# Performance work log

Measured on AMD Instinct MI355X. Metric: run time of the kernel, lower is better.

## Reference

```python
import jax, jax.numpy as jnp
import numpy as np

# Model dims
B, S, D = 1, 768, 256          # batch, seq_len, d_model
H, KD = 8, 256                 # num_heads, key_dim
DH = KD // H                   # head_dim = 32
BS, NR, W, G = 64, 3, 3, 1     # block_size, num_rand_blocks, window_size, global_tokens
NEG = -1e9


def _build_sparse_indices(seed=0):
    """Replicates _create_sparse_attention_mask (sparse branch) with numpy.
    Returns (attn_indices [S, M] int32 clamped >=0, blocked_mask [1,1,S,M] float32)."""
    nb = S // BS  # num_blocks (S divisible by BS here)
    rng = np.random.RandomState(seed)
    r = np.arange(nb)
    # window pairs |i - j| <= W
    ii, jj = np.meshgrid(r, r, indexing='ij')
    win = np.abs(ii - jj) <= W
    window_pairs = np.stack([ii[win], jj[win]], axis=1)
    # global: every block -> first G blocks; first G blocks -> every block
    g = np.arange(G)
    glob_to = np.stack([np.repeat(r, G), np.tile(g, nb)], axis=1)
    glob_from = np.stack([np.repeat(g, nb), np.tile(r, G)], axis=1)
    # random pairs
    rand_pairs = rng.randint(0, nb, size=(NR * nb, 2))
    allp = np.concatenate([window_pairs, glob_to, glob_from, rand_pairs], axis=0)
    uniq = np.unique(allp[:, 0] * nb + allp[:, 1])  # sorted unique (row, col)
    rows, cols = uniq // nb, uniq % nb
    max_row = int(np.max(np.bincount(rows, minlength=nb)))
    M = max_row * BS  # padded neighbor-token width (= S when a global block is dense)
    idx = np.full((nb, M), -1, dtype=np.int64)
    for b in range(nb):
        cs = cols[rows == b]
        toks = (cs[:, None] * BS + np.arange(BS)[None, :]).reshape(-1)
        idx[b, :toks.size] = toks
    tok_idx = idx[np.arange(S) // BS]  # expand per-block rows to per-token rows [S, M]
    mask = np.where(tok_idx >= 0, 0.0, NEG).astype(np.float32)
    return np.maximum(tok_idx, 0).astype(np.int32), mask[None, None]


def setup_inputs() -> dict:
    key = jax.random.key(0)
    ks = jax.random.split(key, 8)

    def dense_w(k, fi, fo):  # glorot-uniform like keras Dense
        lim = float(np.sqrt(6.0 / (fi + fo)))
        return jax.random.uniform(k, (fi, fo), jnp.float32, -lim, lim)

    attn_indices, blocked_mask = _build_sparse_indices()
    return {
        'query': jax.random.normal(ks[0], (B, S, D), jnp.float32),
        'value': jax.random.normal(ks[1], (B, S, D), jnp.float32),
        'key_in': jax.random.normal(ks[2], (B, S, D), jnp.float32),
        'Wq': dense_w(ks[3], D, KD), 'bq': jnp.zeros((KD,), jnp.float32),
        'Wk': dense_w(ks[4], D, KD), 'bk': jnp.zeros((KD,), jnp.float32),
        'Wv': dense_w(ks[5], D, KD), 'bv': jnp.zeros((KD,), jnp.float32),
        'Wo': dense_w(ks[6], KD, D), 'bo': jnp.zeros((D,), jnp.float32),
        'attn_indices': jnp.asarray(attn_indices),
        'blocked_mask': jnp.asarray(blocked_mask),
    }


def reference(query, value, key_in, Wq, bq, Wk, bk, Wv, bv, Wo, bo, attn_indices, blocked_mask):
    q = query @ Wq + bq
    k = key_in @ Wk + bk
    v = value @ Wv + bv

    def split_heads(x):  # [B,S,KD] -> [B*H,S,DH]
        return x.reshape(B, S, H, DH).transpose(0, 2, 1, 3).reshape(B * H, S, DH)

    q = split_heads(q) * (DH ** -0.5)
    k = split_heads(k)
    v = split_heads(v)

    # gather sparse neighbor tokens (indices shared across batch*heads)
    k_g = jnp.take(k, attn_indices, axis=1)  # [BH, S, M, DH]
    v_g = jnp.take(v, attn_indices, axis=1)  # [BH, S, M, DH]

    scores = jnp.einsum('bnd,bnmd->bnm', q, k_g)  # [BH, S, M]
    M = attn_indices.shape[1]
    scores = scores.reshape(B, H, S, M) + blocked_mask  # pad positions -> -1e9
    probs = jax.nn.softmax(scores, axis=-1)

    ctx = jnp.einsum('bnm,bnmd->bnd', probs.reshape(B * H, S, M), v_g)  # [BH,S,DH]
    ctx = ctx.reshape(B, H, S, DH).transpose(0, 2, 1, 3).reshape(B, S, KD)
    out = ctx @ Wo + bo
    return out, scores, attn_indices
```

## Files before the change

### kernel.cpp

```cpp
#include <hip/hip_runtime.h>
#include <math.h>

#define SQ 768
#define DMODEL 256
#define NH 8
#define DHD 32
#define NB 12
#define QSCALE 0.1767766952966369f
#define PSHIFT 8.0f

__global__ __launch_bounds__(256) void proj3(
    const float* __restrict__ query, const float* __restrict__ value,
    const float* __restrict__ key_in,
    const float* __restrict__ Wq, const float* __restrict__ bq,
    const float* __restrict__ Wk, const float* __restrict__ bk,
    const float* __restrict__ Wv, const float* __restrict__ bv,
    const float* __restrict__ bo, float* __restrict__ outbuf,
    const int* __restrict__ aidx, float* __restrict__ idx_out,
    float* __restrict__ qhp, float* __restrict__ khp, float* __restrict__ vhp)
{
    const int j = threadIdx.x;

    {
        const int bidf = blockIdx.y * 192 + blockIdx.x;
        const int i0 = (bidf * 256 + j) * 4;
        int4 v = *(const int4*)&aidx[i0];
        *(float4*)&idx_out[i0] =
            make_float4((float)v.x, (float)v.y, (float)v.z, (float)v.w);
    }

    const int s0 = blockIdx.x * 4;
    const int w  = blockIdx.y;

    if (w == 0) {
        const float bb = bo[j];
        #pragma unroll
        for (int r = 0; r < 4; ++r)
            outbuf[(s0 + r) * DMODEL + j] = bb;
    }

    const float *X, *W, *bias; float* out; float scale;
    if (w == 0)      { X = query;  W = Wq; bias = bq; out = qhp; scale = QSCALE; }
    else if (w == 1) { X = key_in; W = Wk; bias = bk; out = khp; scale = 1.0f; }
    else             { X = value;  W = Wv; bias = bv; out = vhp; scale = 1.0f; }

    __shared__ float xs[4][DMODEL];
    for (int i = j; i < 4 * DMODEL; i += 256)
        xs[i >> 8][i & 255] = X[s0 * DMODEL + i];
    __syncthreads();

    float acc[4] = {};
    #pragma unroll 4
    for (int k = 0; k < DMODEL; ++k) {
        const float wv = W[k * DMODEL + j];
        #pragma unroll
        for (int r = 0; r < 4; ++r)
            acc[r] = fmaf(xs[r][k], wv, acc[r]);
    }
    const float bb = bias[j];
    const int h = j >> 5, d = j & 31;
    #pragma unroll
    for (int r = 0; r < 4; ++r)
        out[h * (SQ * DHD) + (s0 + r) * DHD + d] = (acc[r] + bb) * scale;
}

__global__ __launch_bounds__(512) void attn2(
    const float* __restrict__ qh, const float* __restrict__ kh,
    const float* __restrict__ vh, const int* __restrict__ aidx,
    const float* __restrict__ mask, const float* __restrict__ Wo,
    float* __restrict__ scores_out, float* __restrict__ out, int M)
{
    __shared__ __align__(16) float Qs[32][33];
    __shared__ __align__(16) float Ks[2][32][68];
    __shared__ __align__(16) float Ps[2][64][33];
    __shared__ __align__(16) float Vs[2][64][36];
    __shared__ float invL[32];

    const int b    = blockIdx.x;
    const int half = blockIdx.y;
    const int h    = blockIdx.z;
    const int s0b  = b * 64;
    const int s0   = s0b + half * 32;
    const int tid  = threadIdx.x;
    const int u    = tid >> 8;
    const int utid = tid & 255;
    const int NCH  = M / 64;

    #pragma unroll
    for (int g = 0; g < 2; ++g) {
        const int idx = tid + g * 512;
        const int r = idx >> 5, d = idx & 31;
        Qs[d][r] = qh[(h * SQ + s0 + r) * DHD + d];
    }

    float4 acc = make_float4(0.f, 0.f, 0.f, 0.f);
    float rps = 0.f;
    const int pr  = utid & 31;
    const int pd  = (utid >> 5) * 4;
    const int qrt = (utid & 15) * 2;
    const int qct = (utid >> 4) * 4;

    for (int ci = 0; ci < NCH / 2; ++ci) {
        const int ch = u * (NCH / 2) + ci;
        const int m0 = ch * 64;
        const float maskv = mask[s0b * M + m0];
        const bool valid = maskv > -0.5f;

        __syncthreads();
        if (valid) {
            const int t0 = aidx[s0b * M + m0];
            const int c = utid & 63;
            #pragma unroll
            for (int g = 0; g < 2; ++g) {
                const int d4 = ((utid >> 6) + g * 4) * 4;
                float4 kv = *(const float4*)&kh[(h * SQ + t0 + c) * DHD + d4];
                Ks[u][d4 + 0][c] = kv.x; Ks[u][d4 + 1][c] = kv.y;
                Ks[u][d4 + 2][c] = kv.z; Ks[u][d4 + 3][c] = kv.w;
                *(float4*)&Vs[u][c][d4] =
                    *(const float4*)&vh[(h * SQ + t0 + c) * DHD + d4];
            }
        } else if (utid < 32) {
            float dt = 0.f;
            #pragma unroll
            for (int d = 0; d < 32; ++d)
                dt = fmaf(Qs[d][utid], kh[h * SQ * DHD + d], dt);
            Ps[u][0][utid] = dt;
        }
        __syncthreads();

        if (valid) {
            float sc[2][4] = {};
            #pragma unroll
            for (int kk = 0; kk < 32; ++kk) {
                const float a0 = Qs[kk][qrt];
                const float a1 = Qs[kk][qrt + 1];
                float4 b4 = *(const float4*)&Ks[u][kk][qct];
                sc[0][0] = fmaf(a0, b4.x, sc[0][0]);
                sc[0][1] = fmaf(a0, b4.y, sc[0][1]);
                sc[0][2] = fmaf(a0, b4.z, sc[0][2]);
                sc[0][3] = fmaf(a0, b4.w, sc[0][3]);
                sc[1][0] = fmaf(a1, b4.x, sc[1][0]);
                sc[1][1] = fmaf(a1, b4.y, sc[1][1]);
                sc[1][2] = fmaf(a1, b4.z, sc[1][2]);
                sc[1][3] = fmaf(a1, b4.w, sc[1][3]);
            }
            #pragma unroll
            for (int i = 0; i < 2; ++i) {
                *(float4*)&scores_out[(h * SQ + s0 + qrt + i) * M + m0 + qct] =
                    make_float4(sc[i][0], sc[i][1], sc[i][2], sc[i][3]);
                #pragma unroll
                for (int jj = 0; jj < 4; ++jj)
                    Ps[u][qct + jj][qrt + i] = __expf(sc[i][jj] - PSHIFT);
            }
        } else {
            const float dv = maskv;
            #pragma unroll
            for (int i = 0; i < 8; ++i) {
                const int e = utid + i * 256;
                const int r = e >> 6, cc = e & 63;
                scores_out[(h * SQ + s0 + r) * M + m0 + cc] = Ps[u][0][r] + dv;
            }
        }
        __syncthreads();

        if (valid) {
            #pragma unroll 4
            for (int c = 0; c < 64; ++c) {
                const float p = Ps[u][c][pr];
                float4 v = *(const float4*)&Vs[u][c][pd];
                acc.x = fmaf(p, v.x, acc.x);
                acc.y = fmaf(p, v.y, acc.y);
                acc.z = fmaf(p, v.z, acc.z);
                acc.w = fmaf(p, v.w, acc.w);
                if (utid < 32) rps += p;
            }
        }
    }

    __syncthreads();
    *(float4*)&Vs[u][pr][pd] = acc;
    if (utid < 32) (&Ps[1][0][0])[u * 32 + utid] = rps;
    __syncthreads();

    if (tid < 32) {
        const float pt = (&Ps[1][0][0])[tid] + (&Ps[1][0][0])[32 + tid];
        invL[tid] = 1.0f / pt;
    }
    __syncthreads();

    float* ctxn = &Ks[0][0][0];
    #pragma unroll
    for (int g = 0; g < 2; ++g) {
        const int idx = tid + g * 512;
        const int r = idx >> 5, d = idx & 31;
        ctxn[r * 36 + d] = (Vs[0][r][d] + Vs[1][r][d]) * invL[r];
    }
    __syncthreads();

    {
        const int jc = tid & 255, rg = tid >> 8;
        float wo[32];
        #pragma unroll
        for (int k = 0; k < 32; ++k)
            wo[k] = Wo[(h * DHD + k) * DMODEL + jc];
        for (int rr = rg * 16; rr < rg * 16 + 16; ++rr) {
            float a = 0.f;
            #pragma unroll
            for (int k4 = 0; k4 < 8; ++k4) {
                float4 cv = *(const float4*)&ctxn[rr * 36 + k4 * 4];
                a = fmaf(cv.x, wo[k4 * 4 + 0], a);
                a = fmaf(cv.y, wo[k4 * 4 + 1], a);
                a = fmaf(cv.z, wo[k4 * 4 + 2], a);
                a = fmaf(cv.w, wo[k4 * 4 + 3], a);
            }
            atomicAdd(&out[(s0 + rr) * DMODEL + jc], a);
        }
    }
}

extern "C" void kernel_launch(void* const* d_in, const int* in_sizes, int n_in,
                              void* d_out, int out_size, void* d_ws, size_t ws_size,
                              hipStream_t stream)
{
    const float* query  = (const float*)d_in[0];
    const float* value  = (const float*)d_in[1];
    const float* key_in = (const float*)d_in[2];
    const float* Wq = (const float*)d_in[3];
    const float* bq = (const float*)d_in[4];
    const float* Wk = (const float*)d_in[5];
    const float* bk = (const float*)d_in[6];
    const float* Wv = (const float*)d_in[7];
    const float* bv = (const float*)d_in[8];
    const float* Wo = (const float*)d_in[9];
    const float* bo = (const float*)d_in[10];
    const int*   aidx = (const int*)d_in[11];
    const float* mask = (const float*)d_in[12];

    const int M = in_sizes[11] / SQ;

    float* out        = (float*)d_out;
    float* scores_out = out + SQ * DMODEL;
    float* idx_out    = scores_out + NH * SQ * M;

    float* ws  = (float*)d_ws;
    float* qhp = ws;
    float* khp = qhp + NH * SQ * DHD;
    float* vhp = khp + NH * SQ * DHD;

    proj3<<<dim3(192, 3), 256, 0, stream>>>(
        query, value, key_in, Wq, bq, Wk, bk, Wv, bv,
        bo, out, aidx, idx_out, qhp, khp, vhp);

    attn2<<<dim3(NB, 2, NH), 512, 0, stream>>>(
        qhp, khp, vhp, aidx, mask, Wo, scores_out, out, M);
}
```

Before: 56.54 us.

## Double-buffer K/V chunks in attention, hold Q in registers, widen projection rows

The attention kernel now prefetches the next 64-token K/V chunk into registers while the current chunk is computed, with double-buffered shared memory, and drops one barrier per chunk. Q rows move from shared memory into registers, and the padded-row dot product is computed once up front. The projection kernel processes 8 rows per block, reading X directly as float4 from global instead of staging it in shared memory, which halves the grid. This raises register pressure and leaves fewer, larger projection blocks, which may hurt occupancy.

After: 75.82 us. 1.34x slower.

```diff
diff --git a/kernel.cpp b/kernel.cpp
--- a/kernel.cpp
+++ b/kernel.cpp
@@ -22,46 +22,53 @@
     const int j = threadIdx.x;
 
     {
-        const int bidf = blockIdx.y * 192 + blockIdx.x;
-        const int i0 = (bidf * 256 + j) * 4;
-        int4 v = *(const int4*)&aidx[i0];
+        const int bidf = blockIdx.y * 96 + blockIdx.x;
+        const int i0 = (bidf * 256 + j) * 8;
+        int4 a = *(const int4*)&aidx[i0];
+        int4 b = *(const int4*)&aidx[i0 + 4];
         *(float4*)&idx_out[i0] =
-            make_float4((float)v.x, (float)v.y, (float)v.z, (float)v.w);
-    }
-
-    const int s0 = blockIdx.x * 4;
+            make_float4((float)a.x, (float)a.y, (float)a.z, (float)a.w);
+        *(float4*)&idx_out[i0 + 4] =
+            make_float4((float)b.x, (float)b.y, (float)b.z, (float)b.w);
+    }
+
+    const int s0 = blockIdx.x * 8;
     const int w  = blockIdx.y;
 
     if (w == 0) {
         const float bb = bo[j];
         #pragma unroll
-        for (int r = 0; r < 4; ++r)
+        for (int r = 0; r < 8; ++r)
             outbuf[(s0 + r) * DMODEL + j] = bb;
     }
 
-    const float *X, *W, *bias; float* out; float scale;
-    if (w == 0)      { X = query;  W = Wq; bias = bq; out = qhp; scale = QSCALE; }
-    else if (w == 1) { X = key_in; W = Wk; bias = bk; out = khp; scale = 1.0f; }
-    else             { X = value;  W = Wv; bias = bv; out = vhp; scale = 1.0f; }
-
-    __shared__ float xs[4][DMODEL];
-    for (int i = j; i < 4 * DMODEL; i += 256)
-        xs[i >> 8][i & 255] = X[s0 * DMODEL + i];
-    __syncthreads();
-
-    float acc[4] = {};
-    #pragma unroll 4
-    for (int k = 0; k < DMODEL; ++k) {
-        const float wv = W[k * DMODEL + j];
-        #pragma unroll
-        for (int r = 0; r < 4; ++r)
-            acc[r] = fmaf(xs[r][k], wv, acc[r]);
+    const float *X, *W, *bias; float* outp; float scale;
+    if (w == 0)      { X = query;  W = Wq; bias = bq; outp = qhp; scale = QSCALE; }
+    else if (w == 1) { X = key_in; W = Wk; bias = bk; outp = khp; scale = 1.0f; }
+    else             { X = value;  W = Wv; bias = bv; outp = vhp; scale = 1.0f; }
+
+    const float4* Xv = (const float4*)(X + s0 * DMODEL);
+    float acc[8] = {};
+    for (int k4 = 0; k4 < DMODEL / 4; ++k4) {
+        float xr[8][4];
+        #pragma unroll
+        for (int r = 0; r < 8; ++r) {
+            float4 t = Xv[r * (DMODEL / 4) + k4];
+            xr[r][0] = t.x; xr[r][1] = t.y; xr[r][2] = t.z; xr[r][3] = t.w;
+        }
+        #pragma unroll
+        for (int kk = 0; kk < 4; ++kk) {
+            const float wv = W[(k4 * 4 + kk) * DMODEL + j];
+            #pragma unroll
+            for (int r = 0; r < 8; ++r)
+                acc[r] = fmaf(xr[r][kk], wv, acc[r]);
+        }
     }
     const float bb = bias[j];
     const int h = j >> 5, d = j & 31;
     #pragma unroll
-    for (int r = 0; r < 4; ++r)
-        out[h * (SQ * DHD) + (s0 + r) * DHD + d] = (acc[r] + bb) * scale;
+    for (int r = 0; r < 8; ++r)
+        outp[h * (SQ * DHD) + (s0 + r) * DHD + d] = (acc[r] + bb) * scale;
 }
 
 __global__ __launch_bounds__(512) void attn2(
@@ -70,10 +77,10 @@
     const float* __restrict__ mask, const float* __restrict__ Wo,
     float* __restrict__ scores_out, float* __restrict__ out, int M)
 {
-    __shared__ __align__(16) float Qs[32][33];
-    __shared__ __align__(16) float Ks[2][32][68];
+    __shared__ __align__(16) float Ks[2][2][32][68];
+    __shared__ __align__(16) float Vs[2][2][64][36];
     __shared__ __align__(16) float Ps[2][64][33];
-    __shared__ __align__(16) float Vs[2][64][36];
+    __shared__ float dot0s[32];
     __shared__ float invL[32];
 
     const int b    = blockIdx.x;
@@ -84,90 +91,134 @@
     const int tid  = threadIdx.x;
     const int u    = tid >> 8;
     const int utid = tid & 255;
-    const int NCH  = M / 64;
-
-    #pragma unroll
-    for (int g = 0; g < 2; ++g) {
-        const int idx = tid + g * 512;
-        const int r = idx >> 5, d = idx & 31;
-        Qs[d][r] = qh[(h * SQ + s0 + r) * DHD + d];
-    }
+    const int NCH2 = M / 128;
+
+    const int qrt = (utid & 15) * 2;
+    const int qct = (utid >> 4) * 4;
+    const int pr  = utid & 31;
+    const int pd  = (utid >> 5) * 4;
+    const int c   = utid & 63;
+    const int dg  = utid >> 6;
+    const int d4a = dg * 4;
+    const int d4b = 16 + dg * 4;
+
+    const float* mrow = &mask[s0b * M];
+    const int*   arow = &aidx[s0b * M];
+    float*       srow = &scores_out[(h * SQ + s0) * M];
+
+    float qr0[32], qr1[32];
+    {
+        const float* qp = &qh[(h * SQ + s0 + qrt) * DHD];
+        #pragma unroll
+        for (int d4 = 0; d4 < DHD; d4 += 4) {
+            float4 a  = *(const float4*)&qp[d4];
+            float4 b4 = *(const float4*)&qp[DHD + d4];
+            qr0[d4] = a.x;  qr0[d4+1] = a.y;  qr0[d4+2] = a.z;  qr0[d4+3] = a.w;
+            qr1[d4] = b4.x; qr1[d4+1] = b4.y; qr1[d4+2] = b4.z; qr1[d4+3] = b4.w;
+        }
+    }
+
+    if (tid < 16) {
+        const float* k0 = &kh[h * SQ * DHD];
+        float a0 = 0.f, a1 = 0.f;
+        #pragma unroll
+        for (int d = 0; d < DHD; ++d) {
+            const float kv = k0[d];
+            a0 = fmaf(qr0[d], kv, a0);
+            a1 = fmaf(qr1[d], kv, a1);
+        }
+        dot0s[qrt] = a0; dot0s[qrt + 1] = a1;
+    }
+
+    float mv_cur = mrow[(u * NCH2) * 64];
+    bool  val_cur = mv_cur > -0.5f;
+    if (val_cur) {
+        const int t0 = arow[(u * NCH2) * 64];
+        const float* kp = &kh[(h * SQ + t0 + c) * DHD];
+        const float* vp = &vh[(h * SQ + t0 + c) * DHD];
+        float4 ka = *(const float4*)&kp[d4a];
+        float4 kb = *(const float4*)&kp[d4b];
+        Ks[u][0][d4a+0][c] = ka.x; Ks[u][0][d4a+1][c] = ka.y;
+        Ks[u][0][d4a+2][c] = ka.z; Ks[u][0][d4a+3][c] = ka.w;
+        Ks[u][0][d4b+0][c] = kb.x; Ks[u][0][d4b+1][c] = kb.y;
+        Ks[u][0][d4b+2][c] = kb.z; Ks[u][0][d4b+3][c] = kb.w;
+        *(float4*)&Vs[u][0][c][d4a] = *(const float4*)&vp[d4a];
+        *(float4*)&Vs[u][0][c][d4b] = *(const float4*)&vp[d4b];
+    }
+    __syncthreads();
 
     float4 acc = make_float4(0.f, 0.f, 0.f, 0.f);
     float rps = 0.f;
-    const int pr  = utid & 31;
-    const int pd  = (utid >> 5) * 4;
-    const int qrt = (utid & 15) * 2;
-    const int qct = (utid >> 4) * 4;
-
-    for (int ci = 0; ci < NCH / 2; ++ci) {
-        const int ch = u * (NCH / 2) + ci;
-        const int m0 = ch * 64;
-        const float maskv = mask[s0b * M + m0];
-        const bool valid = maskv > -0.5f;
-
-        __syncthreads();
-        if (valid) {
-            const int t0 = aidx[s0b * M + m0];
-            const int c = utid & 63;
-            #pragma unroll
-            for (int g = 0; g < 2; ++g) {
-                const int d4 = ((utid >> 6) + g * 4) * 4;
-                float4 kv = *(const float4*)&kh[(h * SQ + t0 + c) * DHD + d4];
-                Ks[u][d4 + 0][c] = kv.x; Ks[u][d4 + 1][c] = kv.y;
-                Ks[u][d4 + 2][c] = kv.z; Ks[u][d4 + 3][c] = kv.w;
-                *(float4*)&Vs[u][c][d4] =
-                    *(const float4*)&vh[(h * SQ + t0 + c) * DHD + d4];
-            }
-        } else if (utid < 32) {
-            float dt = 0.f;
-            #pragma unroll
-            for (int d = 0; d < 32; ++d)
-                dt = fmaf(Qs[d][utid], kh[h * SQ * DHD + d], dt);
-            Ps[u][0][utid] = dt;
-        }
-        __syncthreads();
-
-        if (valid) {
+    int cur = 0;
+
+    for (int ci = 0; ci < NCH2; ++ci) {
+        const int m0 = (u * NCH2 + ci) * 64;
+
+        bool  val_nxt = false;
+        float mv_nxt  = 0.f;
+        float4 ka, kb, va, vb;
+        if (ci + 1 < NCH2) {
+            mv_nxt  = mrow[m0 + 64];
+            val_nxt = mv_nxt > -0.5f;
+            if (val_nxt) {
+                const int t0 = arow[m0 + 64];
+                const float* kp = &kh[(h * SQ + t0 + c) * DHD];
+                const float* vp = &vh[(h * SQ + t0 + c) * DHD];
+                ka = *(const float4*)&kp[d4a];
+                kb = *(const float4*)&kp[d4b];
+                va = *(const float4*)&vp[d4a];
+                vb = *(const float4*)&vp[d4b];
+            }
+        }
+
+        if (val_cur) {
+            const float* Kb = &Ks[u][cur][0][qct];
             float sc[2][4] = {};
             #pragma unroll
             for (int kk = 0; kk < 32; ++kk) {
-                const float a0 = Qs[kk][qrt];
-                const float a1 = Qs[kk][qrt + 1];
-                float4 b4 = *(const float4*)&Ks[u][kk][qct];
-                sc[0][0] = fmaf(a0, b4.x, sc[0][0]);
-                sc[0][1] = fmaf(a0, b4.y, sc[0][1]);
-                sc[0][2] = fmaf(a0, b4.z, sc[0][2]);
-                sc[0][3] = fmaf(a0, b4.w, sc[0][3]);
-                sc[1][0] = fmaf(a1, b4.x, sc[1][0]);
-                sc[1][1] = fmaf(a1, b4.y, sc[1][1]);
-                sc[1][2] = fmaf(a1, b4.z, sc[1][2]);
-                sc[1][3] = fmaf(a1, b4.w, sc[1][3]);
+                float4 b4 = *(const float4*)&Kb[kk * 68];
+                sc[0][0] = fmaf(qr0[kk], b4.x, sc[0][0]);
+                sc[0][1] = fmaf(qr0[kk], b4.y, sc[0][1]);
+                sc[0][2] = fmaf(qr0[kk], b4.z, sc[0][2]);
+                sc[0][3] = fmaf(qr0[kk], b4.w, sc[0][3]);
+                sc[1][0] = fmaf(qr1[kk], b4.x, sc[1][0]);
+                sc[1][1] = fmaf(qr1[kk], b4.y, sc[1][1]);
+                sc[1][2] = fmaf(qr1[kk], b4.z, sc[1][2]);
+                sc[1][3] = fmaf(qr1[kk], b4.w, sc[1][3]);
             }
             #pragma unroll
             for (int i = 0; i < 2; ++i) {
-                *(float4*)&scores_out[(h * SQ + s0 + qrt + i) * M + m0 + qct] =
+                *(float4*)&srow[(qrt + i) * M + m0 + qct] =
                     make_float4(sc[i][0], sc[i][1], sc[i][2], sc[i][3]);
                 #pragma unroll
                 for (int jj = 0; jj < 4; ++jj)
                     Ps[u][qct + jj][qrt + i] = __expf(sc[i][jj] - PSHIFT);
             }
         } else {
-            const float dv = maskv;
             #pragma unroll
             for (int i = 0; i < 8; ++i) {
                 const int e = utid + i * 256;
                 const int r = e >> 6, cc = e & 63;
-                scores_out[(h * SQ + s0 + r) * M + m0 + cc] = Ps[u][0][r] + dv;
-            }
+                srow[r * M + m0 + cc] = dot0s[r] + mv_cur;
+            }
+        }
+
+        if (val_nxt) {
+            Ks[u][cur^1][d4a+0][c] = ka.x; Ks[u][cur^1][d4a+1][c] = ka.y;
+            Ks[u][cur^1][d4a+2][c] = ka.z; Ks[u][cur^1][d4a+3][c] = ka.w;
+            Ks[u][cur^1][d4b+0][c] = kb.x; Ks[u][cur^1][d4b+1][c] = kb.y;
+            Ks[u][cur^1][d4b+2][c] = kb.z; Ks[u][cur^1][d4b+3][c] = kb.w;
+            *(float4*)&Vs[u][cur^1][c][d4a] = va;
+            *(float4*)&Vs[u][cur^1][c][d4b] = vb;
         }
         __syncthreads();
 
-        if (valid) {
+        if (val_cur) {
+            const float (*Vb)[36] = Vs[u][cur];
             #pragma unroll 4
-            for (int c = 0; c < 64; ++c) {
-                const float p = Ps[u][c][pr];
-                float4 v = *(const float4*)&Vs[u][c][pd];
+            for (int cc2 = 0; cc2 < 64; ++cc2) {
+                const float p = Ps[u][cc2][pr];
+                float4 v = *(const float4*)&Vb[cc2][pd];
                 acc.x = fmaf(p, v.x, acc.x);
                 acc.y = fmaf(p, v.y, acc.y);
                 acc.z = fmaf(p, v.z, acc.z);
@@ -175,10 +226,12 @@
                 if (utid < 32) rps += p;
             }
         }
-    }
-
-    __syncthreads();
-    *(float4*)&Vs[u][pr][pd] = acc;
+        __syncthreads();
+
+        val_cur = val_nxt; mv_cur = mv_nxt; cur ^= 1;
+    }
+
+    *(float4*)&Vs[u][0][pr][pd] = acc;
     if (utid < 32) (&Ps[1][0][0])[u * 32 + utid] = rps;
     __syncthreads();
 
@@ -188,12 +241,12 @@
     }
     __syncthreads();
 
-    float* ctxn = &Ks[0][0][0];
+    float* ctxn = &Ks[0][0][0][0];
     #pragma unroll
     for (int g = 0; g < 2; ++g) {
         const int idx = tid + g * 512;
         const int r = idx >> 5, d = idx & 31;
-        ctxn[r * 36 + d] = (Vs[0][r][d] + Vs[1][r][d]) * invL[r];
+        ctxn[r * 36 + d] = (Vs[0][0][r][d] + Vs[1][0][r][d]) * invL[r];
     }
     __syncthreads();
 
@@ -247,7 +300,7 @@
     float* khp = qhp + NH * SQ * DHD;
     float* vhp = khp + NH * SQ * DHD;
 
-    proj3<<<dim3(192, 3), 256, 0, stream>>>(
+    proj3<<<dim3(96, 3), 256, 0, stream>>>(
         query, value, key_in, Wq, bq, Wk, bk, Wv, bv,
         bo, out, aidx, idx_out, qhp, khp, vhp);
 
```
